# Optimization experiments

Measured on AMD Instinct MI355X. Metric: run time of the kernel, lower is better.

The kernel has to match this reference:

```python
import jax, jax.numpy as jnp
import numpy as np

KSIZE = 5
STRIDE = 5  # == KSIZE, padding 0: unfold is an exact non-overlapping tiling


def setup_inputs() -> dict:
    key = jax.random.key(0)
    x = jax.random.normal(key, (4, 3, 320, 320), dtype=jnp.float32)
    return {"input": x}


def _extract_patches(x, k):
    # torch.nn.Unfold(k, 1, 0, k) on (n,c,h,w): channel dim ordered (c, ki, kj),
    # spatial positions row-major -> (n, L, c*k*k)
    n, c, h, w = x.shape
    hp, wp = h // k, w // k
    p = x.reshape(n, c, hp, k, wp, k)
    p = jnp.transpose(p, (0, 2, 4, 1, 3, 5))  # (n, hp, wp, c, k, k)
    return p.reshape(n, hp * wp, c * k * k), hp, wp


def reference(input):
    # DotP branch, sigmoid=True, target=None (self-match)
    p, hp, wp = _extract_patches(input, KSIZE)          # (n, L, K)
    n, L, _ = p.shape
    # per-sample scalar: max over patches of patch L2 norm
    max_wi = jnp.max(jnp.sqrt(jnp.sum(p * p, axis=-1)), axis=1)  # (n,)
    # conv2d(xi, wi/max_wi, stride=k) == patch Gram matrix / max_wi
    match = jnp.einsum('bpk,bqk->bpq', p, p) / max_wi[:, None, None]  # (n, L, L)
    match = match.reshape(n, L, hp, wp)
    return jax.nn.sigmoid(match)
```

## Files before the change

### kernel.cpp

```cpp
#include <hip/hip_runtime.h>
#include <hip/hip_bf16.h>

#define NB   4
#define CCH  3
#define HW   320
#define KS   5
#define LP   4096
#define KD   75
#define NCH  12

typedef __attribute__((ext_vector_type(4))) float f32x4;
typedef __attribute__((ext_vector_type(8))) short bf16x8;

__device__ __forceinline__ ushort f2bf(float v) {
    __hip_bfloat16 h = __float2bfloat16(v);
    return __builtin_bit_cast(ushort, h);
}

__global__ __launch_bounds__(256) void patch_kernel(const float* __restrict__ x,
                                                    ushort* __restrict__ p2) {
    int tid = threadIdx.x;
    int r   = blockIdx.x * 256 + tid;
    int c   = blockIdx.y;
    int b   = blockIdx.z;
    int ph = r >> 6, pw = r & 63;
    const float* xb = x + (size_t)b * (CCH * HW * HW);

    bf16x8 v = {};
    if (c < 10) {
        #pragma unroll
        for (int j = 0; j < 8; ++j) {
            int k = c * 8 + j;
            float f = 0.f;
            if (k < KD) {
                int ch = k / 25, rem = k % 25;
                int ki = rem / 5, kj = rem % 5;
                f = xb[(ch * HW + ph * KS + ki) * HW + pw * KS + kj];
            }
            v[j] = (short)f2bf(f);
        }
    }
    *(bf16x8*)&p2[((size_t)(b * NCH + c) * LP + r) * 8] = v;
}

__global__ __launch_bounds__(256) void normb_kernel(const ushort* __restrict__ p2,
                                                    float* __restrict__ blockmax) {
    int b = blockIdx.y;
    int r = blockIdx.x * 256 + threadIdx.x;
    const ushort* pb = p2 + (size_t)b * NCH * LP * 8;

    float ss = 0.f;
    #pragma unroll
    for (int c = 0; c < 10; ++c) {
        bf16x8 v = *(const bf16x8*)&pb[((size_t)c * LP + r) * 8];
        #pragma unroll
        for (int j = 0; j < 8; ++j) {
            float f = __uint_as_float(((unsigned)(ushort)v[j]) << 16);
            ss = fmaf(f, f, ss);
        }
    }
    for (int off = 32; off; off >>= 1) ss = fmaxf(ss, __shfl_xor(ss, off, 64));
    __shared__ float sm[4];
    if ((threadIdx.x & 63) == 0) sm[threadIdx.x >> 6] = ss;
    __syncthreads();
    if (threadIdx.x == 0)
        blockmax[b * 16 + blockIdx.x] =
            fmaxf(fmaxf(sm[0], sm[1]), fmaxf(sm[2], sm[3]));
}

__global__ __launch_bounds__(256) void gemm_kernel(const ushort* __restrict__ p2,
                                                   const float* __restrict__ blockmax,
                                                   float* __restrict__ out) {
    __shared__ float W[32][256];

    int b  = blockIdx.z;
    int ti = blockIdx.x;
    int tj = blockIdx.y;
    int tid = threadIdx.x;
    int lane = tid & 63;
    int w    = tid >> 6;
    int lrow = lane & 15;
    int lch  = lane >> 4;

    const ushort* pb = p2 + (size_t)b * NCH * LP * 8;
    int i0 = ti * 256 + w * 64;
    int j0 = tj * 64;

    f32x4 acc[4][4] = {};
    #pragma unroll
    for (int ks = 0; ks < 3; ++ks) {
        const ushort* pk = pb + (size_t)(ks * 4 + lch) * LP * 8;
        bf16x8 af[4], bfr[4];
        #pragma unroll
        for (int m = 0; m < 4; ++m)
            af[m] = *(const bf16x8*)&pk[(size_t)(i0 + m * 16 + lrow) * 8];
        #pragma unroll
        for (int n = 0; n < 4; ++n)
            bfr[n] = *(const bf16x8*)&pk[(size_t)(j0 + n * 16 + lrow) * 8];
        #pragma unroll
        for (int m = 0; m < 4; ++m)
            #pragma unroll
            for (int n = 0; n < 4; ++n)
                acc[m][n] = __builtin_amdgcn_mfma_f32_16x16x32_bf16(af[m], bfr[n], acc[m][n], 0, 0, 0);
    }

    float mx = 0.f;
    #pragma unroll
    for (int i = 0; i < 16; ++i) mx = fmaxf(mx, blockmax[b * 16 + i]);
    float inv = 1.0f / sqrtf(mx);
    float* ob = out + (size_t)b * LP * LP;

    #pragma unroll
    for (int h = 0; h < 2; ++h) {
        if (h) __syncthreads();
        #pragma unroll
        for (int np = 0; np < 2; ++np) {
            int n  = h * 2 + np;
            int jr = np * 16 + lrow;
            #pragma unroll
            for (int m = 0; m < 4; ++m) {
                int sl = w * 16 + (((m * 4 + lch) ^ (jr & 7)) & 15);
                f32x4 v;
                #pragma unroll
                for (int r = 0; r < 4; ++r) {
                    float s = acc[m][n][r] * inv;
                    v[r] = __builtin_amdgcn_rcpf(1.0f + __expf(-s));
                }
                *(f32x4*)&W[jr][sl * 4] = v;
            }
        }
        __syncthreads();
        #pragma unroll
        for (int r8 = 0; r8 < 8; ++r8) {
            int row = w * 8 + r8;
            f32x4 v = *(const f32x4*)&W[row][(lane ^ (row & 7)) * 4];
            __builtin_nontemporal_store(v,
                (f32x4*)&ob[(size_t)(j0 + h * 32 + row) * LP + ti * 256 + lane * 4]);
        }
    }
}

extern "C" void kernel_launch(void* const* d_in, const int* in_sizes, int n_in,
                              void* d_out, int out_size, void* d_ws, size_t ws_size,
                              hipStream_t stream) {
    const float* x = (const float*)d_in[0];
    float* out = (float*)d_out;

    ushort* p2 = (ushort*)d_ws;
    float* blockmax = (float*)((char*)d_ws + (size_t)NB * NCH * LP * 16);

    patch_kernel<<<dim3(LP / 256, NCH, NB), 256, 0, stream>>>(x, p2);
    normb_kernel<<<dim3(LP / 256, NB), 256, 0, stream>>>(p2, blockmax);
    gemm_kernel<<<dim3(16, 64, NB), 256, 0, stream>>>(p2, blockmax, out);
}
```

Baseline: 61.88 us.

## Give each wave its own 256x16 output strip and drop block barriers in epilogue

```diff
diff --git a/kernel.cpp b/kernel.cpp
--- a/kernel.cpp
+++ b/kernel.cpp
@@ -10,6 +10,7 @@
 #define NCH  12
 
 typedef __attribute__((ext_vector_type(4))) float f32x4;
+typedef __attribute__((ext_vector_type(2))) float f32x2;
 typedef __attribute__((ext_vector_type(8))) short bf16x8;
 
 __device__ __forceinline__ ushort f2bf(float v) {
@@ -71,7 +72,7 @@
 __global__ __launch_bounds__(256) void gemm_kernel(const ushort* __restrict__ p2,
                                                    const float* __restrict__ blockmax,
                                                    float* __restrict__ out) {
-    __shared__ float W[32][256];
+    __shared__ float W[4][16][128];
 
     int b  = blockIdx.z;
     int ti = blockIdx.x;
@@ -83,59 +84,50 @@
     int lch  = lane >> 4;
 
     const ushort* pb = p2 + (size_t)b * NCH * LP * 8;
-    int i0 = ti * 256 + w * 64;
-    int j0 = tj * 64;
+    int i0 = ti * 256;
+    int jw = tj * 64 + w * 16;
 
-    f32x4 acc[4][4] = {};
+    f32x4 acc[16] = {};
     #pragma unroll
     for (int ks = 0; ks < 3; ++ks) {
         const ushort* pk = pb + (size_t)(ks * 4 + lch) * LP * 8;
-        bf16x8 af[4], bfr[4];
+        bf16x8 bfr = *(const bf16x8*)&pk[(size_t)(jw + lrow) * 8];
         #pragma unroll
-        for (int m = 0; m < 4; ++m)
-            af[m] = *(const bf16x8*)&pk[(size_t)(i0 + m * 16 + lrow) * 8];
-        #pragma unroll
-        for (int n = 0; n < 4; ++n)
-            bfr[n] = *(const bf16x8*)&pk[(size_t)(j0 + n * 16 + lrow) * 8];
-        #pragma unroll
-        for (int m = 0; m < 4; ++m)
-            #pragma unroll
-            for (int n = 0; n < 4; ++n)
-                acc[m][n] = __builtin_amdgcn_mfma_f32_16x16x32_bf16(af[m], bfr[n], acc[m][n], 0, 0, 0);
+        for (int m = 0; m < 16; ++m) {
+            bf16x8 af = *(const bf16x8*)&pk[(size_t)(i0 + m * 16 + lrow) * 8];
+            acc[m] = __builtin_amdgcn_mfma_f32_16x16x32_bf16(af, bfr, acc[m], 0, 0, 0);
+        }
     }
 
     float mx = 0.f;
     #pragma unroll
     for (int i = 0; i < 16; ++i) mx = fmaxf(mx, blockmax[b * 16 + i]);
     float inv = 1.0f / sqrtf(mx);
-    float* ob = out + (size_t)b * LP * LP;
 
     #pragma unroll
-    for (int h = 0; h < 2; ++h) {
-        if (h) __syncthreads();
+    for (int m = 0; m < 16; ++m)
         #pragma unroll
-        for (int np = 0; np < 2; ++np) {
-            int n  = h * 2 + np;
-            int jr = np * 16 + lrow;
-            #pragma unroll
-            for (int m = 0; m < 4; ++m) {
-                int sl = w * 16 + (((m * 4 + lch) ^ (jr & 7)) & 15);
-                f32x4 v;
-                #pragma unroll
-                for (int r = 0; r < 4; ++r) {
-                    float s = acc[m][n][r] * inv;
-                    v[r] = __builtin_amdgcn_rcpf(1.0f + __expf(-s));
-                }
-                *(f32x4*)&W[jr][sl * 4] = v;
-            }
+        for (int r = 0; r < 4; ++r)
+            acc[m][r] = __builtin_amdgcn_rcpf(1.0f + __expf(-acc[m][r] * inv));
+
+    float* ob = out + (size_t)b * LP * LP;
+    float* Wp = &W[w][0][0];
+
+    #pragma unroll
+    for (int half = 0; half < 2; ++half) {
+        asm volatile("s_waitcnt lgkmcnt(0)" ::: "memory");
+        #pragma unroll
+        for (int mm = 0; mm < 8; ++mm) {
+            int sl = (mm * 4 + lch) ^ (lrow & 7);
+            *(f32x4*)&Wp[lrow * 128 + sl * 4] = acc[half * 8 + mm];
         }
-        __syncthreads();
+        asm volatile("s_waitcnt lgkmcnt(0)" ::: "memory");
         #pragma unroll
-        for (int r8 = 0; r8 < 8; ++r8) {
-            int row = w * 8 + r8;
-            f32x4 v = *(const f32x4*)&W[row][(lane ^ (row & 7)) * 4];
+        for (int r = 0; r < 16; ++r) {
+            int sl = (lane >> 1) ^ (r & 7);
+            f32x2 v = *(const f32x2*)&Wp[r * 128 + sl * 4 + (lane & 1) * 2];
             __builtin_nontemporal_store(v,
-                (f32x4*)&ob[(size_t)(j0 + h * 32 + row) * LP + ti * 256 + lane * 4]);
+                (f32x2*)&ob[(size_t)(jw + r) * LP + i0 + half * 128 + lane * 2]);
         }
     }
 }
```

Measured after the change: 72.33 us. 16.9% more time.
